# Optimization experiments

Hardware: AMD Instinct MI355X
Metric: run time of the kernel (lower is better)

Reference implementation:

```python
import math
import jax, jax.numpy as jnp
import numpy as np

N = 512
C_S, C_Z, C_H, H, PQ, PV = 384, 128, 16, 12, 4, 8
INF, EPS = 1e5, 1e-8


def _quat_to_rot(q):
    # q: [N,4] unnormalized quaternions -> [N,3,3] rotation matrices
    q = q / jnp.linalg.norm(q, axis=-1, keepdims=True)
    w, x, y, z = q[:, 0], q[:, 1], q[:, 2], q[:, 3]
    return jnp.stack([
        jnp.stack([1 - 2 * (y * y + z * z), 2 * (x * y - w * z), 2 * (x * z + w * y)], -1),
        jnp.stack([2 * (x * y + w * z), 1 - 2 * (x * x + z * z), 2 * (y * z - w * x)], -1),
        jnp.stack([2 * (x * z - w * y), 2 * (y * z + w * x), 1 - 2 * (x * x + y * y)], -1),
    ], -2)


def setup_inputs() -> dict:
    key = jax.random.key(0)
    ks = jax.random.split(key, 16)
    sc = 0.02
    inp = {
        "s": jax.random.normal(ks[0], (N, C_S), jnp.float32),
        "z": jax.random.normal(ks[1], (N, N, C_Z), jnp.float32),
        "rot": _quat_to_rot(jax.random.normal(ks[2], (N, 4), jnp.float32)),
        "trans": jax.random.normal(ks[3], (N, 3), jnp.float32) * 10.0,
        "mask": jnp.ones((N,), jnp.float32),
        "Wq": jax.random.normal(ks[4], (C_S, H * C_H), jnp.float32) * sc,
        "bq": jnp.zeros((H * C_H,), jnp.float32),
        "Wkv": jax.random.normal(ks[5], (C_S, 2 * H * C_H), jnp.float32) * sc,
        "bkv": jnp.zeros((2 * H * C_H,), jnp.float32),
        "Wqp": jax.random.normal(ks[6], (C_S, H * 3 * PQ), jnp.float32) * sc,
        "bqp": jnp.zeros((H * 3 * PQ,), jnp.float32),
        "Wkvp": jax.random.normal(ks[7], (C_S, H * 3 * (PQ + PV)), jnp.float32) * sc,
        "bkvp": jnp.zeros((H * 3 * (PQ + PV),), jnp.float32),
        "Wb": jax.random.normal(ks[8], (C_Z, H), jnp.float32) * sc,
        "bb": jnp.zeros((H,), jnp.float32),
        "head_weights": jnp.full((H,), math.log(math.e - 1.0), jnp.float32),
        "Wout": jax.random.normal(ks[9], (H * (C_Z + C_H + PV * 4), C_S), jnp.float32) * sc,
        "bout": jnp.zeros((C_S,), jnp.float32),
    }
    return inp


def _ipa(s, z, rot, trans, mask, Wq, bq, Wkv, bkv, Wqp, bqp, Wkvp, bkvp, Wb, bb, head_weights, Wout, bout):
    q = (s @ Wq + bq).reshape(N, H, C_H)
    kv = (s @ Wkv + bkv).reshape(N, H, 2 * C_H)
    k, v = kv[..., :C_H], kv[..., C_H:]

    def proj_pts(W, b, P):
        # torch: split last dim into 3 chunks, stack on -1 -> layout [N, 3, H, P] -> [N, H, P, 3]
        pl = (s @ W + b).reshape(N, 3, H, P).transpose(0, 2, 3, 1)
        return jnp.einsum('nij,nhpj->nhpi', rot, pl) + trans[:, None, None, :]

    q_pts = proj_pts(Wqp, bqp, PQ)                    # [N,H,PQ,3]
    kv_pts = proj_pts(Wkvp, bkvp, PQ + PV)            # [N,H,PQ+PV,3]
    k_pts, v_pts = kv_pts[..., :PQ, :], kv_pts[..., PQ:, :]

    b_bias = z @ Wb + bb                              # [N,N,H]
    a = jnp.einsum('ihc,jhc->hij', q, k) * math.sqrt(1.0 / (3 * C_H))
    a = a + math.sqrt(1.0 / 3) * b_bias.transpose(2, 0, 1)

    d2 = jnp.sum((q_pts[:, None] - k_pts[None]) ** 2, axis=-1)   # [i,j,H,PQ]
    hw = jax.nn.softplus(head_weights) * math.sqrt(1.0 / (3 * (PQ * 9.0 / 2)))
    pt_att = -0.5 * jnp.sum(d2 * hw[None, None, :, None], axis=-1)  # [i,j,H]

    sq_mask = INF * (mask[:, None] * mask[None, :] - 1.0)
    a = jax.nn.softmax(a + pt_att.transpose(2, 0, 1) + sq_mask[None], axis=-1)  # [H,i,j]

    o = jnp.einsum('hij,jhc->ihc', a, v).reshape(N, H * C_H)
    o_pt = jnp.einsum('hij,jhpc->ihpc', a, v_pts)                 # [i,H,PV,3]
    o_pt = jnp.einsum('nji,nhpj->nhpi', rot, o_pt - trans[:, None, None, :])  # invert_apply
    o_pt_norm = jnp.sqrt(jnp.sum(o_pt ** 2, axis=-1) + EPS).reshape(N, H * PV)
    o_pt_flat = o_pt.reshape(N, H * PV, 3)
    o_pair = jnp.einsum('hij,ijc->ihc', a, z).reshape(N, H * C_Z)

    cat = jnp.concatenate(
        [o, o_pt_flat[..., 0], o_pt_flat[..., 1], o_pt_flat[..., 2], o_pt_norm, o_pair], axis=-1)
    return cat @ Wout + bout


def reference(s, z, rot, trans, mask, Wq, bq, Wkv, bkv, Wqp, bqp, Wkvp, bkvp, Wb, bb, head_weights, Wout, bout):
    return _ipa(s, z, rot, trans, mask, Wq, bq, Wkv, bkv, Wqp, bqp, Wkvp, bkvp, Wb, bb, head_weights, Wout, bout)
```

## Files before the change

### kernel.cpp

```cpp
#include <hip/hip_runtime.h>
#include <math.h>

#define NN 512
#define CS 384
#define CZ 128
#define CH 16
#define HH 12
#define PQ 4
#define PV 8
#define LGS_S 516

typedef float f32x4 __attribute__((ext_vector_type(4)));
typedef __bf16 bf16x8 __attribute__((ext_vector_type(8)));

__global__ void k_repack(const float* __restrict__ Wq,  const float* __restrict__ bq,
                         const float* __restrict__ Wkv, const float* __restrict__ bkv,
                         const float* __restrict__ Wqp, const float* __restrict__ bqp,
                         const float* __restrict__ Wkvp,const float* __restrict__ bkvp,
                         float* __restrict__ Wcat, float* __restrict__ bcat)
{
    const int total = CS * 1152;
    for (int idx = blockIdx.x * blockDim.x + threadIdx.x; idx < total; idx += gridDim.x * blockDim.x) {
        int kk = idx / 1152, n = idx % 1152;
        float vv;
        if (n < 192)      vv = Wq  [kk * 192 + n];
        else if (n < 576) vv = Wkv [kk * 384 + (n - 192)];
        else if (n < 720) vv = Wqp [kk * 144 + (n - 576)];
        else              vv = Wkvp[kk * 432 + (n - 720)];
        Wcat[idx] = vv;
    }
    int n = blockIdx.x * blockDim.x + threadIdx.x;
    if (n < 1152) {
        float vv;
        if (n < 192)      vv = bq  [n];
        else if (n < 576) vv = bkv [n - 192];
        else if (n < 720) vv = bqp [n - 576];
        else              vv = bkvp[n - 720];
        bcat[n] = vv;
    }
}

__global__ void k_proj(const float* __restrict__ s, const float* __restrict__ Wcat,
                       const float* __restrict__ bcat,
                       float* __restrict__ q, float* __restrict__ k_t, float* __restrict__ v,
                       float* __restrict__ qp_raw, float* __restrict__ kvp_raw)
{
    __shared__ float As[16 * 68];
    __shared__ float Bs[64 * 64];

    int tx = threadIdx.x & 15;
    int ty = threadIdx.x >> 4;
    int n0 = blockIdx.x * 64;
    int m0 = blockIdx.y * 16;

    float acc[4] = {0.f, 0.f, 0.f, 0.f};

    for (int kb = 0; kb < CS; kb += 64) {
        #pragma unroll
        for (int e = 0; e < 4; ++e) {
            int idx = e * 256 + threadIdx.x;
            int m = idx >> 6, kk = idx & 63;
            As[m * 68 + kk] = s[(size_t)(m0 + m) * CS + kb + kk];
        }
        #pragma unroll
        for (int e = 0; e < 16; ++e) {
            int idx = e * 256 + threadIdx.x;
            int kk = idx >> 6, n = idx & 63;
            Bs[kk * 64 + n] = Wcat[(size_t)(kb + kk) * 1152 + n0 + n];
        }
        __syncthreads();

        for (int kk = 0; kk < 64; kk += 4) {
            f32x4 a = *(const f32x4*)&As[ty * 68 + kk];
            f32x4 b[4];
            #pragma unroll
            for (int kq = 0; kq < 4; ++kq)
                b[kq] = *(const f32x4*)&Bs[(kk + kq) * 64 + tx * 4];
            #pragma unroll
            for (int kq = 0; kq < 4; ++kq)
                #pragma unroll
                for (int cc = 0; cc < 4; ++cc)
                    acc[cc] += a[kq] * b[kq][cc];
        }
        __syncthreads();
    }

    int i = m0 + ty;
    #pragma unroll
    for (int cc = 0; cc < 4; ++cc) {
        int col = n0 + tx * 4 + cc;
        float val = acc[cc] + bcat[col];
        if (col < 192) {
            q[i * 192 + col] = val;
        } else if (col < 576) {
            int lc = col - 192;
            int h = lc / 32, w = lc % 32;
            if (w < CH) k_t[(h * CH + w) * NN + i] = val;
            else        v[(i * HH + h) * CH + (w - CH)] = val;
        } else if (col < 720) {
            qp_raw[i * 144 + (col - 576)] = val;
        } else {
            kvp_raw[i * 432 + (col - 720)] = val;
        }
    }
}

__global__ void k_pts_transform(const float* __restrict__ qp_raw, const float* __restrict__ kvp_raw,
                                const float* __restrict__ rot, const float* __restrict__ trans,
                                float* __restrict__ q_pts, float* __restrict__ k_pts_t,
                                float* __restrict__ v_pts)
{
    int idx = blockIdx.x * blockDim.x + threadIdx.x;
    const int total = NN * HH * 16;
    if (idx >= total) return;
    int i = idx / (HH * 16);
    int r = idx % (HH * 16);
    int h = r / 16;
    int p = r % 16;

    float R[9], t3[3];
    for (int a = 0; a < 9; ++a) R[a] = rot[i * 9 + a];
    for (int a = 0; a < 3; ++a) t3[a] = trans[i * 3 + a];

    float x, y, zc;
    if (p < PQ) {
        x  = qp_raw[i * 144 + 0 * 48 + h * PQ + p];
        y  = qp_raw[i * 144 + 1 * 48 + h * PQ + p];
        zc = qp_raw[i * 144 + 2 * 48 + h * PQ + p];
    } else {
        int pp = p - PQ;
        x  = kvp_raw[i * 432 + 0 * 144 + h * 12 + pp];
        y  = kvp_raw[i * 432 + 1 * 144 + h * 12 + pp];
        zc = kvp_raw[i * 432 + 2 * 144 + h * 12 + pp];
    }
    float ox = R[0] * x + R[1] * y + R[2] * zc + t3[0];
    float oy = R[3] * x + R[4] * y + R[5] * zc + t3[1];
    float oz = R[6] * x + R[7] * y + R[8] * zc + t3[2];

    if (p < PQ) {
        int o = ((i * HH + h) * PQ + p) * 3;
        q_pts[o] = ox; q_pts[o + 1] = oy; q_pts[o + 2] = oz;
    } else {
        int pp = p - PQ;
        if (pp < PQ) {
            int rb = (h * PQ + pp) * 3;
            k_pts_t[(size_t)(rb + 0) * NN + i] = ox;
            k_pts_t[(size_t)(rb + 1) * NN + i] = oy;
            k_pts_t[(size_t)(rb + 2) * NN + i] = oz;
        } else {
            int o = ((i * HH + h) * PV + (pp - PQ)) * 3;
            v_pts[o] = ox; v_pts[o + 1] = oy; v_pts[o + 2] = oz;
        }
    }
}

__global__ void __launch_bounds__(512, 4)
k_attn(const float* __restrict__ z, const float* __restrict__ Wb,
       const float* __restrict__ bb,
       const float* __restrict__ q, const float* __restrict__ k_t,
       const float* __restrict__ q_pts, const float* __restrict__ k_pts_t,
       const float* __restrict__ head_weights, const float* __restrict__ mask,
       const float* __restrict__ v, const float* __restrict__ v_pts,
       const float* __restrict__ rot, const float* __restrict__ trans,
       float* __restrict__ cat)
{
    __shared__ float lgs[HH][LGS_S];
    __shared__ float q_lds[HH * CH];
    __shared__ float qp_lds[HH * PQ * 3];
    __shared__ float hw_lds[HH];
    __shared__ float bb_l[HH];
    __shared__ float opt_lds[HH * PV * 3];

    const int i = blockIdx.x;
    const int tid = threadIdx.x;
    const int lane = tid & 63;
    const int wave = tid >> 6;
    const float* zbase = z + (size_t)i * NN * CZ;

    if (tid < HH * CH)     q_lds[tid]  = q[(size_t)i * HH * CH + tid];
    if (tid < HH * PQ * 3) qp_lds[tid] = q_pts[(size_t)i * HH * PQ * 3 + tid];
    if (tid < HH) {
        float x = head_weights[tid];
        hw_lds[tid] = log1pf(expf(x)) * 0.13608276348795434f;
        bb_l[tid] = bb[tid];
    }

    {
        const float b_scale = 0.57735026918962576f;
        const int hcol = lane & 15;
        const int q8 = (lane >> 4) * 8;
        bf16x8 wbf[4];
        #pragma unroll
        for (int kc = 0; kc < 4; ++kc) {
            #pragma unroll
            for (int jj = 0; jj < 8; ++jj) {
                int c = kc * 32 + q8 + jj;
                float wv = (hcol < HH) ? Wb[c * HH + hcol] * b_scale : 0.0f;
                wbf[kc][jj] = (__bf16)wv;
            }
        }
        #pragma unroll
        for (int t = 0; t < 4; ++t) {
            int j0 = (wave * 4 + t) * 16;
            const float* zrow = zbase + (size_t)(j0 + hcol) * CZ;
            f32x4 acc = {0.f, 0.f, 0.f, 0.f};
            #pragma unroll
            for (int kc = 0; kc < 4; ++kc) {
                float4 z0 = *(const float4*)(zrow + kc * 32 + q8);
                float4 z1 = *(const float4*)(zrow + kc * 32 + q8 + 4);
                bf16x8 afrag;
                afrag[0] = (__bf16)z0.x; afrag[1] = (__bf16)z0.y;
                afrag[2] = (__bf16)z0.z; afrag[3] = (__bf16)z0.w;
                afrag[4] = (__bf16)z1.x; afrag[5] = (__bf16)z1.y;
                afrag[6] = (__bf16)z1.z; afrag[7] = (__bf16)z1.w;
                acc = __builtin_amdgcn_mfma_f32_16x16x32_bf16(afrag, wbf[kc], acc, 0, 0, 0);
            }
            if (hcol < HH) {
                #pragma unroll
                for (int r = 0; r < 4; ++r) {
                    int j = j0 + (lane >> 4) * 4 + r;
                    lgs[hcol][j] = acc[r];
                }
            }
        }
    }
    __syncthreads();

    {
        const float qk_scale = 0.14433756729740643f;
        const float b_scale  = 0.57735026918962576f;
        const float sqm = 100000.0f * (mask[i] * mask[tid] - 1.0f);
        #pragma unroll
        for (int h = 0; h < HH; ++h) {
            float accq = 0.f;
            #pragma unroll
            for (int c = 0; c < CH; ++c)
                accq += q_lds[h * CH + c] * k_t[(size_t)(h * CH + c) * NN + tid];
            float s2 = 0.f;
            #pragma unroll
            for (int p = 0; p < PQ; ++p) {
                int rb = (h * PQ + p) * 3;
                float dx = qp_lds[rb + 0] - k_pts_t[(size_t)(rb + 0) * NN + tid];
                float dy = qp_lds[rb + 1] - k_pts_t[(size_t)(rb + 1) * NN + tid];
                float dz = qp_lds[rb + 2] - k_pts_t[(size_t)(rb + 2) * NN + tid];
                s2 += dx * dx + dy * dy + dz * dz;
            }
            lgs[h][tid] += accq * qk_scale + b_scale * bb_l[h] - 0.5f * hw_lds[h] * s2 + sqm;
        }
    }
    __syncthreads();

    for (int row = wave; row < HH; row += 8) {
        float vals[8];
        float m = -1e30f;
        #pragma unroll
        for (int u = 0; u < 8; ++u) { vals[u] = lgs[row][lane + u * 64]; m = fmaxf(m, vals[u]); }
        #pragma unroll
        for (int off = 32; off >= 1; off >>= 1) m = fmaxf(m, __shfl_xor(m, off));
        float ssum = 0.f;
        #pragma unroll
        for (int u = 0; u < 8; ++u) { vals[u] = expf(vals[u] - m); ssum += vals[u]; }
        #pragma unroll
        for (int off = 32; off >= 1; off >>= 1) ssum += __shfl_xor(ssum, off);
        float inv = 1.0f / ssum;
        #pragma unroll
        for (int u = 0; u < 8; ++u) lgs[row][lane + u * 64] = vals[u] * inv;
    }
    __syncthreads();

    if (tid < 480) {
        float acc = 0.f;
        if (tid < 192) {
            const float* lr = lgs[tid >> 4];
            const float* vp = v + tid;
            #pragma unroll 4
            for (int j = 0; j < NN; ++j)
                acc += lr[j] * vp[(size_t)j * 192];
            cat[(size_t)i * 2112 + tid] = acc;
        } else {
            int r = tid - 192;
            const float* lr = lgs[r / 24];
            const float* vp = v_pts + r;
            #pragma unroll 4
            for (int j = 0; j < NN; ++j)
                acc += lr[j] * vp[(size_t)j * 288];
            opt_lds[r] = acc;
        }
    }

    {
        int cl = lane & 15;
        int q4 = lane >> 4;
        int ha = (cl < HH) ? cl : (HH - 1);
        int cb = wave * 16 + cl;
        f32x4 pacc = {0.f, 0.f, 0.f, 0.f};
        for (int ks = 0; ks < 16; ++ks) {
            int jb = ks * 32 + q4 * 8;
            f32x4 a0 = *(const f32x4*)&lgs[ha][jb];
            f32x4 a1 = *(const f32x4*)&lgs[ha][jb + 4];
            bf16x8 af;
            af[0] = (__bf16)a0[0]; af[1] = (__bf16)a0[1];
            af[2] = (__bf16)a0[2]; af[3] = (__bf16)a0[3];
            af[4] = (__bf16)a1[0]; af[5] = (__bf16)a1[1];
            af[6] = (__bf16)a1[2]; af[7] = (__bf16)a1[3];
            bf16x8 bf;
            #pragma unroll
            for (int jj = 0; jj < 8; ++jj)
                bf[jj] = (__bf16)zbase[(size_t)(jb + jj) * CZ + cb];
            pacc = __builtin_amdgcn_mfma_f32_16x16x32_bf16(af, bf, pacc, 0, 0, 0);
        }
        float* crow = cat + (size_t)i * 2112 + 576;
        #pragma unroll
        for (int r = 0; r < 4; ++r) {
            int h = q4 * 4 + r;
            if (h < HH) crow[h * CZ + cb] = pacc[r];
        }
    }
    __syncthreads();

    if (tid < HH * PV) {
        int hp = tid;
        float R[9], t3[3];
        #pragma unroll
        for (int a2 = 0; a2 < 9; ++a2) R[a2] = rot[i * 9 + a2];
        #pragma unroll
        for (int a2 = 0; a2 < 3; ++a2) t3[a2] = trans[i * 3 + a2];
        float gx = opt_lds[hp * 3 + 0] - t3[0];
        float gy = opt_lds[hp * 3 + 1] - t3[1];
        float gz = opt_lds[hp * 3 + 2] - t3[2];
        float lx = R[0] * gx + R[3] * gy + R[6] * gz;
        float ly = R[1] * gx + R[4] * gy + R[7] * gz;
        float lz = R[2] * gx + R[5] * gy + R[8] * gz;
        float* crow = cat + (size_t)i * 2112;
        crow[192 + 0 * 96 + hp] = lx;
        crow[192 + 1 * 96 + hp] = ly;
        crow[192 + 2 * 96 + hp] = lz;
        crow[480 + hp] = sqrtf(lx * lx + ly * ly + lz * lz + 1e-8f);
    }
}

__global__ void k_final(const float* __restrict__ cat, const float* __restrict__ Wout,
                        const float* __restrict__ bout, float* __restrict__ out)
{
    __shared__ float As[16 * 52];
    __shared__ float Bs[48 * 64];

    int tx = threadIdx.x & 15;
    int ty = threadIdx.x >> 4;
    int n0 = blockIdx.x * 64;
    int m0 = blockIdx.y * 16;
    int k0 = blockIdx.z * 528;

    float acc[4] = {0.f, 0.f, 0.f, 0.f};

    for (int stage = 0; stage < 11; ++stage) {
        int kb = k0 + stage * 48;
        #pragma unroll
        for (int e = 0; e < 3; ++e) {
            int idx = e * 256 + threadIdx.x;
            int m = idx / 48, kk = idx % 48;
            As[m * 52 + kk] = cat[(size_t)(m0 + m) * 2112 + kb + kk];
        }
        #pragma unroll
        for (int e = 0; e < 12; ++e) {
            int idx = e * 256 + threadIdx.x;
            int kk = idx >> 6, n = idx & 63;
            Bs[kk * 64 + n] = Wout[(size_t)(kb + kk) * 384 + n0 + n];
        }
        __syncthreads();

        for (int kk = 0; kk < 48; kk += 4) {
            f32x4 a = *(const f32x4*)&As[ty * 52 + kk];
            f32x4 b[4];
            #pragma unroll
            for (int kq = 0; kq < 4; ++kq)
                b[kq] = *(const f32x4*)&Bs[(kk + kq) * 64 + tx * 4];
            #pragma unroll
            for (int kq = 0; kq < 4; ++kq)
                #pragma unroll
                for (int cc = 0; cc < 4; ++cc)
                    acc[cc] += a[kq] * b[kq][cc];
        }
        __syncthreads();
    }

    bool add_bias = (blockIdx.z == 0);
    int m = m0 + ty;
    #pragma unroll
    for (int cc = 0; cc < 4; ++cc) {
        int n = n0 + tx * 4 + cc;
        float val = acc[cc] + (add_bias ? bout[n] : 0.f);
        atomicAdd(&out[(size_t)m * 384 + n], val);
    }
}

extern "C" void kernel_launch(void* const* d_in, const int* in_sizes, int n_in,
                              void* d_out, int out_size, void* d_ws, size_t ws_size,
                              hipStream_t stream)
{
    const float* s     = (const float*)d_in[0];
    const float* z     = (const float*)d_in[1];
    const float* rot   = (const float*)d_in[2];
    const float* trans = (const float*)d_in[3];
    const float* mask  = (const float*)d_in[4];
    const float* Wq    = (const float*)d_in[5];
    const float* bq    = (const float*)d_in[6];
    const float* Wkv   = (const float*)d_in[7];
    const float* bkv   = (const float*)d_in[8];
    const float* Wqp   = (const float*)d_in[9];
    const float* bqp   = (const float*)d_in[10];
    const float* Wkvp  = (const float*)d_in[11];
    const float* bkvp  = (const float*)d_in[12];
    const float* Wb    = (const float*)d_in[13];
    const float* bb    = (const float*)d_in[14];
    const float* hw    = (const float*)d_in[15];
    const float* Wout  = (const float*)d_in[16];
    const float* bout  = (const float*)d_in[17];
    float* out = (float*)d_out;

    float* ws = (float*)d_ws;
    float* q       = ws;
    float* k_t     = ws + 98304;
    float* v       = ws + 196608;
    float* qp_raw  = ws + 294912;
    float* kvp_raw = ws + 368640;
    float* q_pts   = ws + 589824;
    float* k_pts_t = ws + 663552;
    float* v_pts   = ws + 737280;
    float* cat     = ws + 884736;
    float* Wcat    = ws + 1966080;
    float* bcat    = ws + 2408448;

    hipMemsetAsync(out, 0, (size_t)NN * CS * sizeof(float), stream);

    hipLaunchKernelGGL(k_repack, dim3(512), dim3(256), 0, stream,
                       Wq, bq, Wkv, bkv, Wqp, bqp, Wkvp, bkvp, Wcat, bcat);
    hipLaunchKernelGGL(k_proj, dim3(18, 32), dim3(256), 0, stream,
                       s, Wcat, bcat, q, k_t, v, qp_raw, kvp_raw);
    hipLaunchKernelGGL(k_pts_transform, dim3(384), dim3(256), 0, stream,
                       qp_raw, kvp_raw, rot, trans, q_pts, k_pts_t, v_pts);
    hipLaunchKernelGGL(k_attn, dim3(NN), dim3(512), 0, stream,
                       z, Wb, bb, q, k_t, q_pts, k_pts_t, hw, mask,
                       v, v_pts, rot, trans, cat);
    hipLaunchKernelGGL(k_final, dim3(6, 32, 4), dim3(256), 0, stream, cat, Wout, bout, out);
}
```

Measured before the change: 349.4 us.

## Split attention blocks across head halves and split PV reduction over keys

Each query row's attention is now handled by two blocks of six heads each, doubling the grid size and raising the launch-bounds occupancy hint. The value and point-value reductions are split over two key halves, with partial sums combined through shared memory. A block-wide barrier is replaced with a per-wave LDS wait, which is valid because each wave reads only the logits columns it wrote. The aim is more parallelism and less per-block latency. The cost is that each z row is now read by two blocks, and more of the pair-MFMA lanes do padded work.

Result: slower. 386.1 us (+10.5%).

```diff
diff --git a/kernel.cpp b/kernel.cpp
--- a/kernel.cpp
+++ b/kernel.cpp
@@ -154,7 +154,7 @@
     }
 }
 
-__global__ void __launch_bounds__(512, 4)
+__global__ void __launch_bounds__(512, 8)
 k_attn(const float* __restrict__ z, const float* __restrict__ Wb,
        const float* __restrict__ bb,
        const float* __restrict__ q, const float* __restrict__ k_t,
@@ -164,14 +164,16 @@
        const float* __restrict__ rot, const float* __restrict__ trans,
        float* __restrict__ cat)
 {
-    __shared__ float lgs[HH][LGS_S];
+    __shared__ float lgs[6][LGS_S];
     __shared__ float q_lds[HH * CH];
     __shared__ float qp_lds[HH * PQ * 3];
     __shared__ float hw_lds[HH];
     __shared__ float bb_l[HH];
-    __shared__ float opt_lds[HH * PV * 3];
-
-    const int i = blockIdx.x;
+    __shared__ float part_lds[480];
+    __shared__ float opt_lds[6 * PV * 3];
+
+    const int i = blockIdx.x >> 1;
+    const int hbase = (blockIdx.x & 1) * 6;
     const int tid = threadIdx.x;
     const int lane = tid & 63;
     const int wave = tid >> 6;
@@ -184,6 +186,8 @@
         hw_lds[tid] = log1pf(expf(x)) * 0.13608276348795434f;
         bb_l[tid] = bb[tid];
     }
+    const float sqm = 100000.0f * (mask[i] * mask[tid] - 1.0f);
+    __syncthreads();
 
     {
         const float b_scale = 0.57735026918962576f;
@@ -195,7 +199,7 @@
             #pragma unroll
             for (int jj = 0; jj < 8; ++jj) {
                 int c = kc * 32 + q8 + jj;
-                float wv = (hcol < HH) ? Wb[c * HH + hcol] * b_scale : 0.0f;
+                float wv = (hcol < 6) ? Wb[c * HH + hbase + hcol] * b_scale : 0.0f;
                 wbf[kc][jj] = (__bf16)wv;
             }
         }
@@ -215,7 +219,7 @@
                 afrag[6] = (__bf16)z1.z; afrag[7] = (__bf16)z1.w;
                 acc = __builtin_amdgcn_mfma_f32_16x16x32_bf16(afrag, wbf[kc], acc, 0, 0, 0);
             }
-            if (hcol < HH) {
+            if (hcol < 6) {
                 #pragma unroll
                 for (int r = 0; r < 4; ++r) {
                     int j = j0 + (lane >> 4) * 4 + r;
@@ -224,33 +228,36 @@
             }
         }
     }
-    __syncthreads();
+
+    asm volatile("s_waitcnt lgkmcnt(0)" ::: "memory");
+    __builtin_amdgcn_sched_barrier(0);
 
     {
         const float qk_scale = 0.14433756729740643f;
         const float b_scale  = 0.57735026918962576f;
-        const float sqm = 100000.0f * (mask[i] * mask[tid] - 1.0f);
-        #pragma unroll
-        for (int h = 0; h < HH; ++h) {
+        #pragma unroll
+        for (int lh = 0; lh < 6; ++lh) {
+            int g = hbase + lh;
             float accq = 0.f;
             #pragma unroll
             for (int c = 0; c < CH; ++c)
-                accq += q_lds[h * CH + c] * k_t[(size_t)(h * CH + c) * NN + tid];
+                accq += q_lds[g * CH + c] * k_t[(size_t)(g * CH + c) * NN + tid];
             float s2 = 0.f;
             #pragma unroll
             for (int p = 0; p < PQ; ++p) {
-                int rb = (h * PQ + p) * 3;
+                int rb = (g * PQ + p) * 3;
                 float dx = qp_lds[rb + 0] - k_pts_t[(size_t)(rb + 0) * NN + tid];
                 float dy = qp_lds[rb + 1] - k_pts_t[(size_t)(rb + 1) * NN + tid];
                 float dz = qp_lds[rb + 2] - k_pts_t[(size_t)(rb + 2) * NN + tid];
                 s2 += dx * dx + dy * dy + dz * dz;
             }
-            lgs[h][tid] += accq * qk_scale + b_scale * bb_l[h] - 0.5f * hw_lds[h] * s2 + sqm;
+            lgs[lh][tid] += accq * qk_scale + b_scale * bb_l[g] - 0.5f * hw_lds[g] * s2 + sqm;
         }
     }
     __syncthreads();
 
-    for (int row = wave; row < HH; row += 8) {
+    if (wave < 6) {
+        int row = wave;
         float vals[8];
         float m = -1e30f;
         #pragma unroll
@@ -269,31 +276,34 @@
     __syncthreads();
 
     if (tid < 480) {
+        int js  = tid / 240;
+        int out = tid % 240;
+        int jb  = js * 256;
         float acc = 0.f;
-        if (tid < 192) {
-            const float* lr = lgs[tid >> 4];
-            const float* vp = v + tid;
-            #pragma unroll 4
-            for (int j = 0; j < NN; ++j)
+        if (out < 96) {
+            const float* lr = lgs[out >> 4];
+            const float* vp = v + hbase * CH + out;
+            #pragma unroll 8
+            for (int j = jb; j < jb + 256; ++j)
                 acc += lr[j] * vp[(size_t)j * 192];
-            cat[(size_t)i * 2112 + tid] = acc;
         } else {
-            int r = tid - 192;
+            int r = out - 96;
             const float* lr = lgs[r / 24];
-            const float* vp = v_pts + r;
-            #pragma unroll 4
-            for (int j = 0; j < NN; ++j)
+            const float* vp = v_pts + hbase * 24 + r;
+            #pragma unroll 8
+            for (int j = jb; j < jb + 256; ++j)
                 acc += lr[j] * vp[(size_t)j * 288];
-            opt_lds[r] = acc;
-        }
+        }
+        part_lds[out + js * 240] = acc;
     }
 
     {
         int cl = lane & 15;
         int q4 = lane >> 4;
-        int ha = (cl < HH) ? cl : (HH - 1);
+        int ha = (cl < 6) ? cl : 5;
         int cb = wave * 16 + cl;
         f32x4 pacc = {0.f, 0.f, 0.f, 0.f};
+        #pragma unroll 2
         for (int ks = 0; ks < 16; ++ks) {
             int jb = ks * 32 + q4 * 8;
             f32x4 a0 = *(const f32x4*)&lgs[ha][jb];
@@ -312,13 +322,23 @@
         float* crow = cat + (size_t)i * 2112 + 576;
         #pragma unroll
         for (int r = 0; r < 4; ++r) {
-            int h = q4 * 4 + r;
-            if (h < HH) crow[h * CZ + cb] = pacc[r];
+            int lh = q4 * 4 + r;
+            if (lh < 6) crow[(hbase + lh) * CZ + cb] = pacc[r];
         }
     }
     __syncthreads();
 
-    if (tid < HH * PV) {
+    if (tid < 240) {
+        float sum = part_lds[tid] + part_lds[tid + 240];
+        if (tid < 96) {
+            cat[(size_t)i * 2112 + hbase * CH + tid] = sum;
+        } else {
+            opt_lds[tid - 96] = sum;
+        }
+    }
+    __syncthreads();
+
+    if (tid < 6 * PV) {
         int hp = tid;
         float R[9], t3[3];
         #pragma unroll
@@ -331,11 +351,12 @@
         float lx = R[0] * gx + R[3] * gy + R[6] * gz;
         float ly = R[1] * gx + R[4] * gy + R[7] * gz;
         float lz = R[2] * gx + R[5] * gy + R[8] * gz;
+        int hpg = hbase * PV + hp;
         float* crow = cat + (size_t)i * 2112;
-        crow[192 + 0 * 96 + hp] = lx;
-        crow[192 + 1 * 96 + hp] = ly;
-        crow[192 + 2 * 96 + hp] = lz;
-        crow[480 + hp] = sqrtf(lx * lx + ly * ly + lz * lz + 1e-8f);
+        crow[192 + 0 * 96 + hpg] = lx;
+        crow[192 + 1 * 96 + hpg] = ly;
+        crow[192 + 2 * 96 + hpg] = lz;
+        crow[480 + hpg] = sqrtf(lx * lx + ly * ly + lz * lz + 1e-8f);
     }
 }
 
@@ -439,7 +460,7 @@
                        s, Wcat, bcat, q, k_t, v, qp_raw, kvp_raw);
     hipLaunchKernelGGL(k_pts_transform, dim3(384), dim3(256), 0, stream,
                        qp_raw, kvp_raw, rot, trans, q_pts, k_pts_t, v_pts);
-    hipLaunchKernelGGL(k_attn, dim3(NN), dim3(512), 0, stream,
+    hipLaunchKernelGGL(k_attn, dim3(NN * 2), dim3(512), 0, stream,
                        z, Wb, bb, q, k_t, q_pts, k_pts_t, hw, mask,
                        v, v_pts, rot, trans, cat);
     hipLaunchKernelGGL(k_final, dim3(6, 32, 4), dim3(256), 0, stream, cat, Wout, bout, out);
```

## Warp-specialize attention kernel: MFMA waves for z work, other waves for logits and values

Applied to the files above, without the earlier changes.

Splits the 8 waves of each block into two groups. Waves 0-3 compute the pair bias via MFMA over twice as many rows, and later the o_pair MFMA with two accumulators. Waves 4-7 meanwhile compute the qk and point-distance logits into registers, and later the v and v_pts reductions. This overlaps memory-heavy z streaming with ALU and global-load work that previously ran serially, at the cost of an extra barrier and more registers per thread.

New measurement: 405.1 us. 1.16x slower.

```diff
diff --git a/kernel.cpp b/kernel.cpp
--- a/kernel.cpp
+++ b/kernel.cpp
@@ -184,8 +184,12 @@
         hw_lds[tid] = log1pf(expf(x)) * 0.13608276348795434f;
         bb_l[tid] = bb[tid];
     }
-
-    {
+    const float mask_i = mask[i];
+    __syncthreads();
+
+    float lgv[2][HH];
+
+    if (wave < 4) {
         const float b_scale = 0.57735026918962576f;
         const int hcol = lane & 15;
         const int q8 = (lane >> 4) * 8;
@@ -199,9 +203,9 @@
                 wbf[kc][jj] = (__bf16)wv;
             }
         }
-        #pragma unroll
-        for (int t = 0; t < 4; ++t) {
-            int j0 = (wave * 4 + t) * 16;
+        #pragma unroll 2
+        for (int t = 0; t < 8; ++t) {
+            int j0 = wave * 128 + t * 16;
             const float* zrow = zbase + (size_t)(j0 + hcol) * CZ;
             f32x4 acc = {0.f, 0.f, 0.f, 0.f};
             #pragma unroll
@@ -223,30 +227,42 @@
                 }
             }
         }
-    }
-    __syncthreads();
-
-    {
+    } else {
         const float qk_scale = 0.14433756729740643f;
         const float b_scale  = 0.57735026918962576f;
-        const float sqm = 100000.0f * (mask[i] * mask[tid] - 1.0f);
-        #pragma unroll
-        for (int h = 0; h < HH; ++h) {
-            float accq = 0.f;
-            #pragma unroll
-            for (int c = 0; c < CH; ++c)
-                accq += q_lds[h * CH + c] * k_t[(size_t)(h * CH + c) * NN + tid];
-            float s2 = 0.f;
-            #pragma unroll
-            for (int p = 0; p < PQ; ++p) {
-                int rb = (h * PQ + p) * 3;
-                float dx = qp_lds[rb + 0] - k_pts_t[(size_t)(rb + 0) * NN + tid];
-                float dy = qp_lds[rb + 1] - k_pts_t[(size_t)(rb + 1) * NN + tid];
-                float dz = qp_lds[rb + 2] - k_pts_t[(size_t)(rb + 2) * NN + tid];
-                s2 += dx * dx + dy * dy + dz * dz;
-            }
-            lgs[h][tid] += accq * qk_scale + b_scale * bb_l[h] - 0.5f * hw_lds[h] * s2 + sqm;
-        }
+        const int tw = tid - 256;
+        #pragma unroll
+        for (int s2i = 0; s2i < 2; ++s2i) {
+            const int j = tw + s2i * 256;
+            const float sqm = 100000.0f * (mask_i * mask[j] - 1.0f);
+            #pragma unroll
+            for (int h = 0; h < HH; ++h) {
+                float accq = 0.f;
+                #pragma unroll
+                for (int c = 0; c < CH; ++c)
+                    accq += q_lds[h * CH + c] * k_t[(size_t)(h * CH + c) * NN + j];
+                float s2 = 0.f;
+                #pragma unroll
+                for (int p = 0; p < PQ; ++p) {
+                    int rb = (h * PQ + p) * 3;
+                    float dx = qp_lds[rb + 0] - k_pts_t[(size_t)(rb + 0) * NN + j];
+                    float dy = qp_lds[rb + 1] - k_pts_t[(size_t)(rb + 1) * NN + j];
+                    float dz = qp_lds[rb + 2] - k_pts_t[(size_t)(rb + 2) * NN + j];
+                    s2 += dx * dx + dy * dy + dz * dz;
+                }
+                lgv[s2i][h] = accq * qk_scale + b_scale * bb_l[h] - 0.5f * hw_lds[h] * s2 + sqm;
+            }
+        }
+    }
+    __syncthreads();
+
+    if (wave >= 4) {
+        const int tw = tid - 256;
+        #pragma unroll
+        for (int s2i = 0; s2i < 2; ++s2i)
+            #pragma unroll
+            for (int h = 0; h < HH; ++h)
+                lgs[h][tw + s2i * 256] += lgv[s2i][h];
     }
     __syncthreads();
 
@@ -268,32 +284,14 @@
     }
     __syncthreads();
 
-    if (tid < 480) {
-        float acc = 0.f;
-        if (tid < 192) {
-            const float* lr = lgs[tid >> 4];
-            const float* vp = v + tid;
-            #pragma unroll 4
-            for (int j = 0; j < NN; ++j)
-                acc += lr[j] * vp[(size_t)j * 192];
-            cat[(size_t)i * 2112 + tid] = acc;
-        } else {
-            int r = tid - 192;
-            const float* lr = lgs[r / 24];
-            const float* vp = v_pts + r;
-            #pragma unroll 4
-            for (int j = 0; j < NN; ++j)
-                acc += lr[j] * vp[(size_t)j * 288];
-            opt_lds[r] = acc;
-        }
-    }
-
-    {
+    if (wave < 4) {
         int cl = lane & 15;
         int q4 = lane >> 4;
         int ha = (cl < HH) ? cl : (HH - 1);
-        int cb = wave * 16 + cl;
-        f32x4 pacc = {0.f, 0.f, 0.f, 0.f};
+        int cb0 = wave * 16 + cl;
+        int cb1 = cb0 + 64;
+        f32x4 p0 = {0.f, 0.f, 0.f, 0.f};
+        f32x4 p1 = {0.f, 0.f, 0.f, 0.f};
         for (int ks = 0; ks < 16; ++ks) {
             int jb = ks * 32 + q4 * 8;
             f32x4 a0 = *(const f32x4*)&lgs[ha][jb];
@@ -303,17 +301,48 @@
             af[2] = (__bf16)a0[2]; af[3] = (__bf16)a0[3];
             af[4] = (__bf16)a1[0]; af[5] = (__bf16)a1[1];
             af[6] = (__bf16)a1[2]; af[7] = (__bf16)a1[3];
-            bf16x8 bf;
-            #pragma unroll
-            for (int jj = 0; jj < 8; ++jj)
-                bf[jj] = (__bf16)zbase[(size_t)(jb + jj) * CZ + cb];
-            pacc = __builtin_amdgcn_mfma_f32_16x16x32_bf16(af, bf, pacc, 0, 0, 0);
+            bf16x8 b0, b1;
+            #pragma unroll
+            for (int jj = 0; jj < 8; ++jj) {
+                b0[jj] = (__bf16)zbase[(size_t)(jb + jj) * CZ + cb0];
+                b1[jj] = (__bf16)zbase[(size_t)(jb + jj) * CZ + cb1];
+            }
+            p0 = __builtin_amdgcn_mfma_f32_16x16x32_bf16(af, b0, p0, 0, 0, 0);
+            p1 = __builtin_amdgcn_mfma_f32_16x16x32_bf16(af, b1, p1, 0, 0, 0);
         }
         float* crow = cat + (size_t)i * 2112 + 576;
         #pragma unroll
         for (int r = 0; r < 4; ++r) {
             int h = q4 * 4 + r;
-            if (h < HH) crow[h * CZ + cb] = pacc[r];
+            if (h < HH) {
+                crow[h * CZ + cb0] = p0[r];
+                crow[h * CZ + cb1] = p1[r];
+            }
+        }
+    } else {
+        const int tw = tid - 256;
+        #pragma unroll
+        for (int pass = 0; pass < 2; ++pass) {
+            int out = tw + pass * 256;
+            if (out < 480) {
+                float acc = 0.f;
+                if (out < 192) {
+                    const float* lr = lgs[out >> 4];
+                    const float* vp = v + out;
+                    #pragma unroll 4
+                    for (int j = 0; j < NN; ++j)
+                        acc += lr[j] * vp[(size_t)j * 192];
+                    cat[(size_t)i * 2112 + out] = acc;
+                } else {
+                    int r = out - 192;
+                    const float* lr = lgs[r / 24];
+                    const float* vp = v_pts + r;
+                    #pragma unroll 4
+                    for (int j = 0; j < NN; ++j)
+                        acc += lr[j] * vp[(size_t)j * 288];
+                    opt_lds[r] = acc;
+                }
+            }
         }
     }
     __syncthreads();
```

## Split attention over four key chunks with flash-style partial softmax combine

Applied to the files above, without the earlier changes.

The attention kernel now runs one block per (query row, key quarter) instead of one per query row. Each block computes its own local max and sum plus unnormalized partial outputs, and a new combine kernel rescales and merges them before the point transform. This raises the block count from 512 to 2048 for more parallelism and better latency hiding. In exchange it adds an extra launch and global round-trips for the partial outputs and stats.

Result: no change. 351.9 us (+0.7%).

```diff
diff --git a/kernel.cpp b/kernel.cpp
--- a/kernel.cpp
+++ b/kernel.cpp
@@ -8,7 +8,6 @@
 #define HH 12
 #define PQ 4
 #define PV 8
-#define LGS_S 516
 
 typedef float f32x4 __attribute__((ext_vector_type(4)));
 typedef __bf16 bf16x8 __attribute__((ext_vector_type(8)));
@@ -154,24 +153,25 @@
     }
 }
 
-__global__ void __launch_bounds__(512, 4)
-k_attn(const float* __restrict__ z, const float* __restrict__ Wb,
-       const float* __restrict__ bb,
-       const float* __restrict__ q, const float* __restrict__ k_t,
-       const float* __restrict__ q_pts, const float* __restrict__ k_pts_t,
-       const float* __restrict__ head_weights, const float* __restrict__ mask,
-       const float* __restrict__ v, const float* __restrict__ v_pts,
-       const float* __restrict__ rot, const float* __restrict__ trans,
-       float* __restrict__ cat)
-{
-    __shared__ float lgs[HH][LGS_S];
+__global__ void __launch_bounds__(512, 8)
+k_attn_part(const float* __restrict__ z, const float* __restrict__ Wb,
+            const float* __restrict__ bb,
+            const float* __restrict__ q, const float* __restrict__ k_t,
+            const float* __restrict__ q_pts, const float* __restrict__ k_pts_t,
+            const float* __restrict__ head_weights, const float* __restrict__ mask,
+            const float* __restrict__ v, const float* __restrict__ v_pts,
+            float* __restrict__ stats, float* __restrict__ part,
+            float* __restrict__ opair)
+{
+    __shared__ float lgs[HH][132];
     __shared__ float q_lds[HH * CH];
     __shared__ float qp_lds[HH * PQ * 3];
     __shared__ float hw_lds[HH];
     __shared__ float bb_l[HH];
-    __shared__ float opt_lds[HH * PV * 3];
-
-    const int i = blockIdx.x;
+
+    const int i  = blockIdx.x >> 2;
+    const int jq = blockIdx.x & 3;
+    const int j0 = jq * 128;
     const int tid = threadIdx.x;
     const int lane = tid & 63;
     const int wave = tid >> 6;
@@ -184,6 +184,8 @@
         hw_lds[tid] = log1pf(expf(x)) * 0.13608276348795434f;
         bb_l[tid] = bb[tid];
     }
+    const float mask_i = mask[i];
+    __syncthreads();
 
     {
         const float b_scale = 0.57735026918962576f;
@@ -199,29 +201,24 @@
                 wbf[kc][jj] = (__bf16)wv;
             }
         }
-        #pragma unroll
-        for (int t = 0; t < 4; ++t) {
-            int j0 = (wave * 4 + t) * 16;
-            const float* zrow = zbase + (size_t)(j0 + hcol) * CZ;
-            f32x4 acc = {0.f, 0.f, 0.f, 0.f};
-            #pragma unroll
-            for (int kc = 0; kc < 4; ++kc) {
-                float4 z0 = *(const float4*)(zrow + kc * 32 + q8);
-                float4 z1 = *(const float4*)(zrow + kc * 32 + q8 + 4);
-                bf16x8 afrag;
-                afrag[0] = (__bf16)z0.x; afrag[1] = (__bf16)z0.y;
-                afrag[2] = (__bf16)z0.z; afrag[3] = (__bf16)z0.w;
-                afrag[4] = (__bf16)z1.x; afrag[5] = (__bf16)z1.y;
-                afrag[6] = (__bf16)z1.z; afrag[7] = (__bf16)z1.w;
-                acc = __builtin_amdgcn_mfma_f32_16x16x32_bf16(afrag, wbf[kc], acc, 0, 0, 0);
-            }
-            if (hcol < HH) {
-                #pragma unroll
-                for (int r = 0; r < 4; ++r) {
-                    int j = j0 + (lane >> 4) * 4 + r;
-                    lgs[hcol][j] = acc[r];
-                }
-            }
+        const int jl0 = wave * 16;
+        const float* zrow = zbase + (size_t)(j0 + jl0 + hcol) * CZ;
+        f32x4 acc = {0.f, 0.f, 0.f, 0.f};
+        #pragma unroll
+        for (int kc = 0; kc < 4; ++kc) {
+            float4 z0 = *(const float4*)(zrow + kc * 32 + q8);
+            float4 z1 = *(const float4*)(zrow + kc * 32 + q8 + 4);
+            bf16x8 afrag;
+            afrag[0] = (__bf16)z0.x; afrag[1] = (__bf16)z0.y;
+            afrag[2] = (__bf16)z0.z; afrag[3] = (__bf16)z0.w;
+            afrag[4] = (__bf16)z1.x; afrag[5] = (__bf16)z1.y;
+            afrag[6] = (__bf16)z1.z; afrag[7] = (__bf16)z1.w;
+            acc = __builtin_amdgcn_mfma_f32_16x16x32_bf16(afrag, wbf[kc], acc, 0, 0, 0);
+        }
+        if (hcol < HH) {
+            #pragma unroll
+            for (int r = 0; r < 4; ++r)
+                lgs[hcol][jl0 + (lane >> 4) * 4 + r] = acc[r];
         }
     }
     __syncthreads();
@@ -229,42 +226,49 @@
     {
         const float qk_scale = 0.14433756729740643f;
         const float b_scale  = 0.57735026918962576f;
-        const float sqm = 100000.0f * (mask[i] * mask[tid] - 1.0f);
-        #pragma unroll
-        for (int h = 0; h < HH; ++h) {
+        const int cl = tid & 127;
+        const int j  = j0 + cl;
+        const int hg = tid >> 7;
+        const float sqm = 100000.0f * (mask_i * mask[j] - 1.0f);
+        #pragma unroll
+        for (int hh = 0; hh < 3; ++hh) {
+            int h = hg * 3 + hh;
             float accq = 0.f;
             #pragma unroll
             for (int c = 0; c < CH; ++c)
-                accq += q_lds[h * CH + c] * k_t[(size_t)(h * CH + c) * NN + tid];
+                accq += q_lds[h * CH + c] * k_t[(size_t)(h * CH + c) * NN + j];
             float s2 = 0.f;
             #pragma unroll
             for (int p = 0; p < PQ; ++p) {
                 int rb = (h * PQ + p) * 3;
-                float dx = qp_lds[rb + 0] - k_pts_t[(size_t)(rb + 0) * NN + tid];
-                float dy = qp_lds[rb + 1] - k_pts_t[(size_t)(rb + 1) * NN + tid];
-                float dz = qp_lds[rb + 2] - k_pts_t[(size_t)(rb + 2) * NN + tid];
+                float dx = qp_lds[rb + 0] - k_pts_t[(size_t)(rb + 0) * NN + j];
+                float dy = qp_lds[rb + 1] - k_pts_t[(size_t)(rb + 1) * NN + j];
+                float dz = qp_lds[rb + 2] - k_pts_t[(size_t)(rb + 2) * NN + j];
                 s2 += dx * dx + dy * dy + dz * dz;
             }
-            lgs[h][tid] += accq * qk_scale + b_scale * bb_l[h] - 0.5f * hw_lds[h] * s2 + sqm;
+            lgs[h][cl] += accq * qk_scale + b_scale * bb_l[h] - 0.5f * hw_lds[h] * s2 + sqm;
         }
     }
     __syncthreads();
 
     for (int row = wave; row < HH; row += 8) {
-        float vals[8];
-        float m = -1e30f;
-        #pragma unroll
-        for (int u = 0; u < 8; ++u) { vals[u] = lgs[row][lane + u * 64]; m = fmaxf(m, vals[u]); }
+        float v0 = lgs[row][lane];
+        float v1 = lgs[row][lane + 64];
+        float m = fmaxf(v0, v1);
         #pragma unroll
         for (int off = 32; off >= 1; off >>= 1) m = fmaxf(m, __shfl_xor(m, off));
-        float ssum = 0.f;
-        #pragma unroll
-        for (int u = 0; u < 8; ++u) { vals[u] = expf(vals[u] - m); ssum += vals[u]; }
-        #pragma unroll
-        for (int off = 32; off >= 1; off >>= 1) ssum += __shfl_xor(ssum, off);
-        float inv = 1.0f / ssum;
-        #pragma unroll
-        for (int u = 0; u < 8; ++u) lgs[row][lane + u * 64] = vals[u] * inv;
+        float e0 = expf(v0 - m);
+        float e1 = expf(v1 - m);
+        float ss = e0 + e1;
+        #pragma unroll
+        for (int off = 32; off >= 1; off >>= 1) ss += __shfl_xor(ss, off);
+        lgs[row][lane]      = e0;
+        lgs[row][lane + 64] = e1;
+        if (lane == 0) {
+            size_t sb = ((size_t)(i * 4 + jq) * HH + row) * 2;
+            stats[sb]     = m;
+            stats[sb + 1] = ss;
+        }
     }
     __syncthreads();
 
@@ -272,20 +276,19 @@
         float acc = 0.f;
         if (tid < 192) {
             const float* lr = lgs[tid >> 4];
-            const float* vp = v + tid;
+            const float* vp = v + (size_t)j0 * 192 + tid;
             #pragma unroll 4
-            for (int j = 0; j < NN; ++j)
+            for (int j = 0; j < 128; ++j)
                 acc += lr[j] * vp[(size_t)j * 192];
-            cat[(size_t)i * 2112 + tid] = acc;
         } else {
             int r = tid - 192;
             const float* lr = lgs[r / 24];
-            const float* vp = v_pts + r;
+            const float* vp = v_pts + (size_t)j0 * 288 + r;
             #pragma unroll 4
-            for (int j = 0; j < NN; ++j)
+            for (int j = 0; j < 128; ++j)
                 acc += lr[j] * vp[(size_t)j * 288];
-            opt_lds[r] = acc;
-        }
+        }
+        part[(size_t)(i * 4 + jq) * 480 + tid] = acc;
     }
 
     {
@@ -294,7 +297,8 @@
         int ha = (cl < HH) ? cl : (HH - 1);
         int cb = wave * 16 + cl;
         f32x4 pacc = {0.f, 0.f, 0.f, 0.f};
-        for (int ks = 0; ks < 16; ++ks) {
+        #pragma unroll
+        for (int ks = 0; ks < 4; ++ks) {
             int jb = ks * 32 + q4 * 8;
             f32x4 a0 = *(const f32x4*)&lgs[ha][jb];
             f32x4 a1 = *(const f32x4*)&lgs[ha][jb + 4];
@@ -306,15 +310,68 @@
             bf16x8 bf;
             #pragma unroll
             for (int jj = 0; jj < 8; ++jj)
-                bf[jj] = (__bf16)zbase[(size_t)(jb + jj) * CZ + cb];
+                bf[jj] = (__bf16)zbase[(size_t)(j0 + jb + jj) * CZ + cb];
             pacc = __builtin_amdgcn_mfma_f32_16x16x32_bf16(af, bf, pacc, 0, 0, 0);
         }
-        float* crow = cat + (size_t)i * 2112 + 576;
         #pragma unroll
         for (int r = 0; r < 4; ++r) {
             int h = q4 * 4 + r;
-            if (h < HH) crow[h * CZ + cb] = pacc[r];
-        }
+            if (h < HH)
+                opair[(size_t)(i * 4 + jq) * 1536 + h * 128 + cb] = pacc[r];
+        }
+    }
+}
+
+__global__ void __launch_bounds__(512, 8)
+k_combine(const float* __restrict__ stats, const float* __restrict__ part,
+          const float* __restrict__ opair,
+          const float* __restrict__ rot, const float* __restrict__ trans,
+          float* __restrict__ cat)
+{
+    __shared__ float f_lds[HH][4];
+    __shared__ float opt_lds[HH * PV * 3];
+
+    const int i = blockIdx.x;
+    const int tid = threadIdx.x;
+
+    if (tid < HH) {
+        float m[4], s[4];
+        #pragma unroll
+        for (int qq = 0; qq < 4; ++qq) {
+            size_t sb = ((size_t)(i * 4 + qq) * HH + tid) * 2;
+            m[qq] = stats[sb];
+            s[qq] = stats[sb + 1];
+        }
+        float M = fmaxf(fmaxf(m[0], m[1]), fmaxf(m[2], m[3]));
+        float Z = 0.f;
+        float e[4];
+        #pragma unroll
+        for (int qq = 0; qq < 4; ++qq) { e[qq] = expf(m[qq] - M); Z += s[qq] * e[qq]; }
+        float invZ = 1.0f / Z;
+        #pragma unroll
+        for (int qq = 0; qq < 4; ++qq) f_lds[tid][qq] = e[qq] * invZ;
+    }
+    __syncthreads();
+
+    if (tid < 480) {
+        int h = (tid < 192) ? (tid >> 4) : ((tid - 192) / 24);
+        float acc = 0.f;
+        #pragma unroll
+        for (int qq = 0; qq < 4; ++qq)
+            acc += f_lds[h][qq] * part[(size_t)(i * 4 + qq) * 480 + tid];
+        if (tid < 192) cat[(size_t)i * 2112 + tid] = acc;
+        else           opt_lds[tid - 192] = acc;
+    }
+
+    #pragma unroll
+    for (int k = 0; k < 3; ++k) {
+        int idx = tid + k * 512;
+        int h = idx >> 7;
+        float acc = 0.f;
+        #pragma unroll
+        for (int qq = 0; qq < 4; ++qq)
+            acc += f_lds[h][qq] * opair[(size_t)(i * 4 + qq) * 1536 + idx];
+        cat[(size_t)i * 2112 + 576 + idx] = acc;
     }
     __syncthreads();
 
@@ -430,6 +487,9 @@
     float* cat     = ws + 884736;
     float* Wcat    = ws + 1966080;
     float* bcat    = ws + 2408448;
+    float* stats   = ws + 2409600;
+    float* part    = ws + 2458752;
+    float* opairb  = ws + 3441792;
 
     hipMemsetAsync(out, 0, (size_t)NN * CS * sizeof(float), stream);
 
@@ -439,8 +499,10 @@
                        s, Wcat, bcat, q, k_t, v, qp_raw, kvp_raw);
     hipLaunchKernelGGL(k_pts_transform, dim3(384), dim3(256), 0, stream,
                        qp_raw, kvp_raw, rot, trans, q_pts, k_pts_t, v_pts);
-    hipLaunchKernelGGL(k_attn, dim3(NN), dim3(512), 0, stream,
+    hipLaunchKernelGGL(k_attn_part, dim3(NN * 4), dim3(512), 0, stream,
                        z, Wb, bb, q, k_t, q_pts, k_pts_t, hw, mask,
-                       v, v_pts, rot, trans, cat);
+                       v, v_pts, stats, part, opairb);
+    hipLaunchKernelGGL(k_combine, dim3(NN), dim3(512), 0, stream,
+                       stats, part, opairb, rot, trans, cat);
     hipLaunchKernelGGL(k_final, dim3(6, 32, 4), dim3(256), 0, stream, cat, Wout, bout, out);
 }
```
